# Performance work log

Measured on AMD Instinct MI355X. Metric: run time of the kernel, lower is better.

## Reference

```python
import jax, jax.numpy as jnp
import numpy as np

N = 100000
IN_DIM = 128
HID = 64
OUT = 4


def _gcn_conv(x, W, b, src, dst, deg_inv_sqrt):
    """PyG GCNConv: linear transform, then symmetric-normalized scatter-add.
    src/dst already include self-loops; deg_inv_sqrt precomputed over them."""
    h = x @ W                                   # [N, H]
    norm = deg_inv_sqrt[src] * deg_inv_sqrt[dst]  # [E+N]
    msg = h[src] * norm[:, None]                # gather + scale, [E+N, H]
    out = jax.ops.segment_sum(msg, dst, num_segments=N)  # scatter-add
    return out + b


def setup_inputs() -> dict:
    key = jax.random.key(0)
    ks = jax.random.split(key, 8)
    E = 1600000
    x = jax.random.normal(ks[0], (N, IN_DIM), dtype=jnp.float32)
    edge_index = jax.random.randint(ks[1], (2, E), 0, N, dtype=jnp.int32)
    # Glorot-ish init for weights
    W1 = jax.random.normal(ks[2], (IN_DIM, HID), dtype=jnp.float32) / np.sqrt(IN_DIM)
    b1 = jnp.zeros((HID,), dtype=jnp.float32)
    W2 = jax.random.normal(ks[3], (HID, HID), dtype=jnp.float32) / np.sqrt(HID)
    b2 = jnp.zeros((HID,), dtype=jnp.float32)
    Wfc = jax.random.normal(ks[4], (HID, OUT), dtype=jnp.float32) / np.sqrt(HID)
    bfc = jnp.zeros((OUT,), dtype=jnp.float32)
    return {"x": x, "edge_index": edge_index, "W1": W1, "b1": b1,
            "W2": W2, "b2": b2, "Wfc": Wfc, "bfc": bfc}


def reference(x, edge_index, W1, b1, W2, b2, Wfc, bfc):
    # Add self-loops (GCNConv default add_self_loops=True)
    loops = jnp.arange(N, dtype=edge_index.dtype)
    src = jnp.concatenate([edge_index[0], loops])
    dst = jnp.concatenate([edge_index[1], loops])
    # Symmetric normalization: deg computed at aggregation targets (dst)
    deg = jax.ops.segment_sum(jnp.ones_like(dst, dtype=x.dtype), dst,
                              num_segments=N)
    deg_inv_sqrt = jnp.where(deg > 0, jax.lax.rsqrt(deg), 0.0)

    h = _gcn_conv(x, W1, b1, src, dst, deg_inv_sqrt)
    h = jax.nn.relu(h)                 # dropout is identity in eval mode
    h = _gcn_conv(h, W2, b2, src, dst, deg_inv_sqrt)
    h = jax.nn.relu(h)
    return h @ Wfc + bfc               # [N, 4]
```

## Files before the change

### kernel.cpp

```cpp
#include <hip/hip_runtime.h>
#include <hip/hip_fp16.h>


#define BCAP 5120
#define BINB 512
#define CHUNK 3200
#define CAP  64
#define LCAP 32

typedef float v2f __attribute__((ext_vector_type(2)));
typedef _Float16 f16x8 __attribute__((ext_vector_type(8)));
typedef float f32x4 __attribute__((ext_vector_type(4)));

__global__ __launch_bounds__(256) void k_bin(const int* __restrict__ src,
                                             const int* __restrict__ dst, int e,
                                             int* bcur, unsigned* __restrict__ binned) {
    __shared__ unsigned ec[CHUNK];
    __shared__ unsigned short eb[CHUNK];
    __shared__ int lh[512], lbase[512], lr[512];
    int t = threadIdx.x;
    for (int i = t; i < 512; i += 256) { lh[i] = 0; lr[i] = 0; }
    __syncthreads();
    int chunk = (e + BINB - 1) / BINB;
    int lo = blockIdx.x * chunk;
    int hi = min(e, lo + chunk);
    for (int i = lo + t; i < hi; i += 256) {
        int d = dst[i];
        int b = d >> 8;
        ec[i - lo] = ((unsigned)src[i] << 8) | (unsigned)(d & 255);
        eb[i - lo] = (unsigned short)b;
        atomicAdd(&lh[b], 1);
    }
    __syncthreads();
    for (int i = t; i < 512; i += 256)
        lbase[i] = lh[i] ? atomicAdd(&bcur[i], lh[i]) : 0;
    __syncthreads();
    int cnt = hi - lo;
    for (int i = t; i < cnt; i += 256) {
        int b = eb[i];
        int r = lbase[b] + atomicAdd(&lr[b], 1);
        if (r < BCAP)
            binned[(size_t)b * BCAP + r] = ec[i];
    }
}

__global__ __launch_bounds__(256) void k_bk2_gemm1(
        const unsigned* __restrict__ binned, const int* __restrict__ bcur,
        int nbk, int* __restrict__ cnt, int* __restrict__ slots,
        const float* __restrict__ X, const float* __restrict__ W1,
        __half* __restrict__ Hh, int n) {
    __shared__ union {
        struct {
            int lists[256 * (LCAP + 1)];
            int lcnt[256];
        } k;
        struct {
            _Float16 As[128 * 136];
            _Float16 Bs[64 * 136];
        } g;
    } sm;

    int t = threadIdx.x;

    if ((int)blockIdx.x < nbk) {
        int b = blockIdx.x;
        int node0 = b << 8;
        size_t ebase = (size_t)b * BCAP;
        int ecnt = min(bcur[b], BCAP);
        sm.k.lcnt[t] = 0;
        __syncthreads();
        for (int j = t; j < ecnt; j += 256) {
            unsigned ed = binned[ebase + j];
            int ld = ed & 255u;
            int s  = (int)(ed >> 8);
            int r  = atomicAdd(&sm.k.lcnt[ld], 1);
            if (r < LCAP)
                sm.k.lists[ld * (LCAP + 1) + r] = s;
            else if (r < CAP)
                slots[((size_t)(node0 + ld) << 6) + r] = s;
        }
        __syncthreads();
        if (node0 + t < n) cnt[node0 + t] = sm.k.lcnt[t];
        for (int k = t; k < 256 * LCAP; k += 256) {
            int ld = k >> 5;
            int r  = k & (LCAP - 1);
            if (r < min(sm.k.lcnt[ld], LCAP) && node0 + ld < n)
                slots[((size_t)(node0 + ld) << 6) + r] =
                    sm.k.lists[ld * (LCAP + 1) + r];
        }
    } else {
        constexpr int K = 128, KP = 136;
        _Float16* As = sm.g.As;
        _Float16* Bs = sm.g.Bs;
        _Float16* H = (_Float16*)Hh;

        #pragma unroll
        for (int p = 0; p < 8; ++p) {
            int i = t + p * 256;
            int k = i >> 4, nn4 = (i & 15) << 2;
            float4 v = ((const float4*)W1)[i];
            Bs[(nn4 + 0) * KP + k] = (_Float16)v.x;
            Bs[(nn4 + 1) * KP + k] = (_Float16)v.y;
            Bs[(nn4 + 2) * KP + k] = (_Float16)v.z;
            Bs[(nn4 + 3) * KP + k] = (_Float16)v.w;
        }

        int row0 = ((int)blockIdx.x - nbk) * 128;
        #pragma unroll
        for (int p = 0; p < 8; ++p) {
            int gi  = t + p * 256;
            int row = gi >> 4, sg = gi & 15;
            int grow = row0 + row;
            float4 v0 = make_float4(0.f, 0.f, 0.f, 0.f), v1 = v0;
            if (grow < n) {
                v0 = *(const float4*)(X + (size_t)grow * K + sg * 8);
                v1 = *(const float4*)(X + (size_t)grow * K + sg * 8 + 4);
            }
            union { __half2 h[4]; float4 f; } u;
            u.h[0] = __floats2half2_rn(v0.x, v0.y);
            u.h[1] = __floats2half2_rn(v0.z, v0.w);
            u.h[2] = __floats2half2_rn(v1.x, v1.y);
            u.h[3] = __floats2half2_rn(v1.z, v1.w);
            *(float4*)(As + row * KP + sg * 8) = u.f;
        }
        __syncthreads();

        int wv   = t >> 6;
        int lane = t & 63;
        int m    = lane & 15;
        int quad = lane >> 4;
        int r0   = wv * 32;

        f32x4 acc[2][4] = {};
        #pragma unroll
        for (int kb = 0; kb < K / 32; ++kb) {
            f16x8 af0 = *(const f16x8*)(As + (r0 + m) * KP + quad * 8 + kb * 32);
            f16x8 af1 = *(const f16x8*)(As + (r0 + 16 + m) * KP + quad * 8 + kb * 32);
            #pragma unroll
            for (int nt = 0; nt < 4; ++nt) {
                f16x8 bf = *(const f16x8*)(Bs + (nt * 16 + m) * KP + quad * 8 + kb * 32);
                acc[0][nt] = __builtin_amdgcn_mfma_f32_16x16x32_f16(af0, bf, acc[0][nt], 0, 0, 0);
                acc[1][nt] = __builtin_amdgcn_mfma_f32_16x16x32_f16(af1, bf, acc[1][nt], 0, 0, 0);
            }
        }

        #pragma unroll
        for (int mt = 0; mt < 2; ++mt) {
            int gr[4];
            #pragma unroll
            for (int r = 0; r < 4; ++r)
                gr[r] = row0 + r0 + mt * 16 + quad * 4 + r;
            #pragma unroll
            for (int nt = 0; nt < 4; ++nt)
                #pragma unroll
                for (int r = 0; r < 4; ++r) {
                    if (gr[r] < n)
                        H[(size_t)gr[r] * 64 + nt * 16 + m] =
                            (_Float16)acc[mt][nt][r];
                    else if (gr[r] == n)
                        H[(size_t)n * 64 + nt * 16 + m] = (_Float16)0.f;
                }
        }
    }
}

__device__ inline void add_row(const __half* __restrict__ hp, int s, int c4,
                               v2f& lo, v2f& hi) {
    float2 raw = *(const float2*)(hp + (size_t)s * 64 + c4);
    const __half2* p = (const __half2*)&raw;
    float2 l = __half22float2(p[0]);
    float2 h = __half22float2(p[1]);
    lo += (v2f){ l.x, l.y };
    hi += (v2f){ h.x, h.y };
}

__device__ inline void fma_row(const __half* __restrict__ hp, int s, int c4,
                               float w, v2f& lo, v2f& hi) {
    float2 raw = *(const float2*)(hp + (size_t)s * 64 + c4);
    const __half2* p = (const __half2*)&raw;
    float2 l = __half22float2(p[0]);
    float2 h = __half22float2(p[1]);
    lo += w * (v2f){ l.x, l.y };
    hi += w * (v2f){ h.x, h.y };
}

__global__ __launch_bounds__(256) void k_gather_mm(const __half* __restrict__ hp,
                                                   const int* __restrict__ slots,
                                                   const int* __restrict__ cnt,
                                                   const float* __restrict__ bias,
                                                   const float* __restrict__ W2,
                                                   __half* __restrict__ h2,
                                                   int n) {
    int lane = threadIdx.x & 63;
    int wid  = (blockIdx.x * blockDim.x + threadIdx.x) >> 6;
    if (wid >= n) return;
    int d    = wid;
    int esub = lane >> 4;
    int c4   = (lane & 15) * 4;

    float w[64];
    #pragma unroll
    for (int k = 0; k < 64; ++k)
        w[k] = W2[k * 64 + lane];

    size_t start = (size_t)d << 6;
    int num = cnt[d];
    int lim = min(num, CAP);
    int idx = (lane < lim) ? slots[start + lane] : 0;
    float dsv = rsqrtf((float)(cnt[idx] + 1));
    float dd  = rsqrtf((float)(num + 1));

    v2f aL[4] = {}, aH[4] = {};
    if (esub == 0)
        fma_row(hp, d, c4, dd, aL[0], aH[0]);

    int j = 0;
    for (; j + 16 <= lim; j += 16) {
        int s0 = __shfl(idx, j + esub);
        int s1 = __shfl(idx, j + 4 + esub);
        int s2 = __shfl(idx, j + 8 + esub);
        int s3 = __shfl(idx, j + 12 + esub);
        float w0 = __shfl(dsv, j + esub);
        float w1 = __shfl(dsv, j + 4 + esub);
        float w2 = __shfl(dsv, j + 8 + esub);
        float w3 = __shfl(dsv, j + 12 + esub);
        fma_row(hp, s0, c4, w0, aL[0], aH[0]);
        fma_row(hp, s1, c4, w1, aL[1], aH[1]);
        fma_row(hp, s2, c4, w2, aL[2], aH[2]);
        fma_row(hp, s3, c4, w3, aL[3], aH[3]);
    }
    for (; j < lim; j += 4) {
        int jj = j + esub;
        int sr = __shfl(idx, jj);
        int s  = (jj < lim) ? sr : n;
        float ww = __shfl(dsv, jj);
        fma_row(hp, s, c4, ww, aL[0], aH[0]);
    }
    v2f sL = (aL[0] + aL[1]) + (aL[2] + aL[3]);
    v2f sH = (aH[0] + aH[1]) + (aH[2] + aH[3]);
    float4 a0 = make_float4(sL.x, sL.y, sH.x, sH.y);
    #pragma unroll
    for (int o = 16; o <= 32; o <<= 1) {
        a0.x += __shfl_xor(a0.x, o);
        a0.y += __shfl_xor(a0.y, o);
        a0.z += __shfl_xor(a0.z, o);
        a0.w += __shfl_xor(a0.w, o);
    }
    float4 bb = *(const float4*)(bias + c4);
    float4 o;
    o.x = fmaxf(bb.x + dd * a0.x, 0.f);
    o.y = fmaxf(bb.y + dd * a0.y, 0.f);
    o.z = fmaxf(bb.z + dd * a0.z, 0.f);
    o.w = fmaxf(bb.w + dd * a0.w, 0.f);

    float s = 0.f;
    #pragma unroll
    for (int kq = 0; kq < 16; ++kq) {
        float ax = __shfl(o.x, kq);
        float ay = __shfl(o.y, kq);
        float az = __shfl(o.z, kq);
        float aw = __shfl(o.w, kq);
        s += ax * w[4 * kq + 0];
        s += ay * w[4 * kq + 1];
        s += az * w[4 * kq + 2];
        s += aw * w[4 * kq + 3];
    }
    _Float16* h2f = (_Float16*)h2;
    h2f[(size_t)d * 64 + lane] = (_Float16)(s * dd);
    if (wid == 0)
        h2f[(size_t)n * 64 + lane] = (_Float16)0.f;
}

__global__ __launch_bounds__(256) void k_gather_fc(const __half* __restrict__ hp,
                                                   const int* __restrict__ slots,
                                                   const int* __restrict__ cnt,
                                                   const float* __restrict__ bias,
                                                   float* __restrict__ outb,
                                                   const float* __restrict__ Wfc,
                                                   const float* __restrict__ bfc,
                                                   int n) {
    int lane = threadIdx.x & 63;
    int wid  = (blockIdx.x * blockDim.x + threadIdx.x) >> 6;
    if (wid >= n) return;
    int d    = wid;
    int esub = lane >> 4;
    int c4   = (lane & 15) * 4;

    size_t start = (size_t)d << 6;
    int num = cnt[d];
    int lim = min(num, CAP);
    int idx = (lane < lim) ? slots[start + lane] : 0;
    float dd = rsqrtf((float)(num + 1));

    v2f aL[4] = {}, aH[4] = {};
    if (esub == 0)
        add_row(hp, d, c4, aL[0], aH[0]);

    int j = 0;
    for (; j + 16 <= lim; j += 16) {
        int s0 = __shfl(idx, j + esub);
        int s1 = __shfl(idx, j + 4 + esub);
        int s2 = __shfl(idx, j + 8 + esub);
        int s3 = __shfl(idx, j + 12 + esub);
        add_row(hp, s0, c4, aL[0], aH[0]);
        add_row(hp, s1, c4, aL[1], aH[1]);
        add_row(hp, s2, c4, aL[2], aH[2]);
        add_row(hp, s3, c4, aL[3], aH[3]);
    }
    for (; j < lim; j += 4) {
        int jj = j + esub;
        int sr = __shfl(idx, jj);
        int s  = (jj < lim) ? sr : n;
        add_row(hp, s, c4, aL[0], aH[0]);
    }
    v2f sL = (aL[0] + aL[1]) + (aL[2] + aL[3]);
    v2f sH = (aH[0] + aH[1]) + (aH[2] + aH[3]);
    float4 a0 = make_float4(sL.x, sL.y, sH.x, sH.y);
    #pragma unroll
    for (int o = 16; o <= 32; o <<= 1) {
        a0.x += __shfl_xor(a0.x, o);
        a0.y += __shfl_xor(a0.y, o);
        a0.z += __shfl_xor(a0.z, o);
        a0.w += __shfl_xor(a0.w, o);
    }
    float4 bb = *(const float4*)(bias + c4);
    float4 o;
    o.x = fmaxf(bb.x + dd * a0.x, 0.f);
    o.y = fmaxf(bb.y + dd * a0.y, 0.f);
    o.z = fmaxf(bb.z + dd * a0.z, 0.f);
    o.w = fmaxf(bb.w + dd * a0.w, 0.f);

    const float4* W4 = (const float4*)Wfc;
    float4 w0 = W4[c4 + 0], w1 = W4[c4 + 1], w2 = W4[c4 + 2], w3 = W4[c4 + 3];
    float4 p;
    p.x = o.x * w0.x + o.y * w1.x + o.z * w2.x + o.w * w3.x;
    p.y = o.x * w0.y + o.y * w1.y + o.z * w2.y + o.w * w3.y;
    p.z = o.x * w0.z + o.y * w1.z + o.z * w2.z + o.w * w3.z;
    p.w = o.x * w0.w + o.y * w1.w + o.z * w2.w + o.w * w3.w;
    #pragma unroll
    for (int q = 1; q <= 8; q <<= 1) {
        p.x += __shfl_xor(p.x, q);
        p.y += __shfl_xor(p.y, q);
        p.z += __shfl_xor(p.z, q);
        p.w += __shfl_xor(p.w, q);
    }
    if (lane == 0) {
        float4 bf = *(const float4*)bfc;
        float4 r = make_float4(p.x + bf.x, p.y + bf.y, p.z + bf.z, p.w + bf.w);
        ((float4*)outb)[d] = r;
    }
}

static inline size_t align256(size_t x) { return (x + 255) & ~(size_t)255; }

extern "C" void kernel_launch(void* const* d_in, const int* in_sizes, int n_in,
                              void* d_out, int out_size, void* d_ws, size_t ws_size,
                              hipStream_t stream) {
    const float* x   = (const float*)d_in[0];
    const int*   ei  = (const int*)d_in[1];
    const float* W1  = (const float*)d_in[2];
    const float* b1  = (const float*)d_in[3];
    const float* W2  = (const float*)d_in[4];
    const float* b2  = (const float*)d_in[5];
    const float* Wfc = (const float*)d_in[6];
    const float* bfc = (const float*)d_in[7];
    float* out = (float*)d_out;

    int n = in_sizes[0] / 128;
    int e = in_sizes[1] / 2;
    const int* src = ei;
    const int* dst = ei + e;

    char* ws = (char*)d_ws;
    size_t p = 0;
    int*      cnt    = (int*)     (ws + p); p = align256(p + (size_t)n * 4);
    int*      bcur   = (int*)     (ws + p); p = align256(p + 512 * 4);
    unsigned* binned = (unsigned*)(ws + p); p = align256(p + (size_t)512 * BCAP * 4);
    int*      slots  = (int*)     (ws + p); p = align256(p + (size_t)n * CAP * 4);
    __half*   hbuf   = (__half*)  (ws + p); p = align256(p + (size_t)(n + 1) * 64 * 2);
    __half*   hbuf2  = (__half*)  (ws + p); p = align256(p + (size_t)(n + 1) * 64 * 2);

    int gb  = (n + 127) / 128;
    int nbk = (n + 255) / 256;

    hipMemsetAsync(bcur, 0, 512 * sizeof(int), stream);
    k_bin<<<BINB, 256, 0, stream>>>(src, dst, e, bcur, binned);
    k_bk2_gemm1<<<nbk + gb, 256, 0, stream>>>(binned, bcur, nbk, cnt, slots,
                                              x, W1, hbuf, n);

    k_gather_mm<<<(n * 64 + 255) / 256, 256, 0, stream>>>(
        hbuf, slots, cnt, b1, W2, hbuf2, n);

    k_gather_fc<<<(n * 64 + 255) / 256, 256, 0, stream>>>(
        hbuf2, slots, cnt, b2, out, Wfc, bfc, n);
}
```

Baseline: 309.2 us.

## Fuse edge binning with GEMM1, use finer buckets, stage W2 in LDS

Moves the edge-binning pass into the same launch as the first GEMM so the two run concurrently. Bucket granularity drops from 256 to 128 destination nodes, giving 784 buckets and a separate 512-thread bucketing kernel. The gather-matmul kernel now stages a transposed W2 in shared memory instead of holding 64 weights per thread in registers, which is meant to cut register pressure and raise occupancy. The trade-offs are an extra block-wide barrier, LDS use, and a per-bucket capacity of 2560 edges, which could drop edges if a bucket overflows.

```diff
diff --git a/kernel.cpp b/kernel.cpp
--- a/kernel.cpp
+++ b/kernel.cpp
@@ -2,9 +2,10 @@
 #include <hip/hip_fp16.h>
 
 
-#define BCAP 5120
+#define BCAP 2560
 #define BINB 512
 #define CHUNK 3200
+#define NBH  784
 #define CAP  64
 #define LCAP 32
 
@@ -12,48 +13,17 @@
 typedef _Float16 f16x8 __attribute__((ext_vector_type(8)));
 typedef float f32x4 __attribute__((ext_vector_type(4)));
 
-__global__ __launch_bounds__(256) void k_bin(const int* __restrict__ src,
-                                             const int* __restrict__ dst, int e,
-                                             int* bcur, unsigned* __restrict__ binned) {
-    __shared__ unsigned ec[CHUNK];
-    __shared__ unsigned short eb[CHUNK];
-    __shared__ int lh[512], lbase[512], lr[512];
-    int t = threadIdx.x;
-    for (int i = t; i < 512; i += 256) { lh[i] = 0; lr[i] = 0; }
-    __syncthreads();
-    int chunk = (e + BINB - 1) / BINB;
-    int lo = blockIdx.x * chunk;
-    int hi = min(e, lo + chunk);
-    for (int i = lo + t; i < hi; i += 256) {
-        int d = dst[i];
-        int b = d >> 8;
-        ec[i - lo] = ((unsigned)src[i] << 8) | (unsigned)(d & 255);
-        eb[i - lo] = (unsigned short)b;
-        atomicAdd(&lh[b], 1);
-    }
-    __syncthreads();
-    for (int i = t; i < 512; i += 256)
-        lbase[i] = lh[i] ? atomicAdd(&bcur[i], lh[i]) : 0;
-    __syncthreads();
-    int cnt = hi - lo;
-    for (int i = t; i < cnt; i += 256) {
-        int b = eb[i];
-        int r = lbase[b] + atomicAdd(&lr[b], 1);
-        if (r < BCAP)
-            binned[(size_t)b * BCAP + r] = ec[i];
-    }
-}
-
-__global__ __launch_bounds__(256) void k_bk2_gemm1(
-        const unsigned* __restrict__ binned, const int* __restrict__ bcur,
-        int nbk, int* __restrict__ cnt, int* __restrict__ slots,
+__global__ __launch_bounds__(256) void k_bin_gemm1(
+        const int* __restrict__ src, const int* __restrict__ dst, int e,
+        int* bcur, unsigned* __restrict__ binned,
         const float* __restrict__ X, const float* __restrict__ W1,
         __half* __restrict__ Hh, int n) {
     __shared__ union {
         struct {
-            int lists[256 * (LCAP + 1)];
-            int lcnt[256];
-        } k;
+            unsigned ec[CHUNK];
+            unsigned short eb[CHUNK];
+            int lh[NBH], lbase[NBH], lr[NBH];
+        } b;
         struct {
             _Float16 As[128 * 136];
             _Float16 Bs[64 * 136];
@@ -62,31 +32,30 @@
 
     int t = threadIdx.x;
 
-    if ((int)blockIdx.x < nbk) {
-        int b = blockIdx.x;
-        int node0 = b << 8;
-        size_t ebase = (size_t)b * BCAP;
-        int ecnt = min(bcur[b], BCAP);
-        sm.k.lcnt[t] = 0;
+    if ((int)blockIdx.x < BINB) {
+        auto& B = sm.b;
+        for (int i = t; i < NBH; i += 256) { B.lh[i] = 0; B.lr[i] = 0; }
         __syncthreads();
-        for (int j = t; j < ecnt; j += 256) {
-            unsigned ed = binned[ebase + j];
-            int ld = ed & 255u;
-            int s  = (int)(ed >> 8);
-            int r  = atomicAdd(&sm.k.lcnt[ld], 1);
-            if (r < LCAP)
-                sm.k.lists[ld * (LCAP + 1) + r] = s;
-            else if (r < CAP)
-                slots[((size_t)(node0 + ld) << 6) + r] = s;
+        int chunk = (e + BINB - 1) / BINB;
+        int lo = blockIdx.x * chunk;
+        int hi = min(e, lo + chunk);
+        for (int i = lo + t; i < hi; i += 256) {
+            int d = dst[i];
+            int b = d >> 7;
+            B.ec[i - lo] = ((unsigned)src[i] << 7) | (unsigned)(d & 127);
+            B.eb[i - lo] = (unsigned short)b;
+            atomicAdd(&B.lh[b], 1);
         }
         __syncthreads();
-        if (node0 + t < n) cnt[node0 + t] = sm.k.lcnt[t];
-        for (int k = t; k < 256 * LCAP; k += 256) {
-            int ld = k >> 5;
-            int r  = k & (LCAP - 1);
-            if (r < min(sm.k.lcnt[ld], LCAP) && node0 + ld < n)
-                slots[((size_t)(node0 + ld) << 6) + r] =
-                    sm.k.lists[ld * (LCAP + 1) + r];
+        for (int i = t; i < NBH; i += 256)
+            B.lbase[i] = B.lh[i] ? atomicAdd(&bcur[i], B.lh[i]) : 0;
+        __syncthreads();
+        int cnt = hi - lo;
+        for (int i = t; i < cnt; i += 256) {
+            int b = B.eb[i];
+            int r = B.lbase[b] + atomicAdd(&B.lr[b], 1);
+            if (r < BCAP)
+                binned[(size_t)b * BCAP + r] = B.ec[i];
         }
     } else {
         constexpr int K = 128, KP = 136;
@@ -105,7 +74,7 @@
             Bs[(nn4 + 3) * KP + k] = (_Float16)v.w;
         }
 
-        int row0 = ((int)blockIdx.x - nbk) * 128;
+        int row0 = ((int)blockIdx.x - BINB) * 128;
         #pragma unroll
         for (int p = 0; p < 8; ++p) {
             int gi  = t + p * 256;
@@ -164,6 +133,39 @@
     }
 }
 
+__global__ __launch_bounds__(512) void k_bucket2(const unsigned* __restrict__ binned,
+                                                 const int* __restrict__ bcur,
+                                                 int n, int* __restrict__ cnt,
+                                                 int* __restrict__ slots) {
+    __shared__ int lists[128 * (LCAP + 1)];
+    __shared__ int lcnt[128];
+    int b = blockIdx.x, t = threadIdx.x;
+    int node0 = b << 7;
+    size_t ebase = (size_t)b * BCAP;
+    int ecnt = min(bcur[b], BCAP);
+    if (t < 128) lcnt[t] = 0;
+    __syncthreads();
+    for (int j = t; j < ecnt; j += 512) {
+        unsigned ed = binned[ebase + j];
+        int ld = ed & 127u;
+        int s  = (int)(ed >> 7);
+        int r  = atomicAdd(&lcnt[ld], 1);
+        if (r < LCAP)
+            lists[ld * (LCAP + 1) + r] = s;
+        else if (r < CAP)
+            slots[((size_t)(node0 + ld) << 6) + r] = s;
+    }
+    __syncthreads();
+    if (t < 128 && node0 + t < n) cnt[node0 + t] = lcnt[t];
+    for (int k = t; k < 128 * LCAP; k += 512) {
+        int ld = k >> 5;
+        int r  = k & (LCAP - 1);
+        if (r < min(lcnt[ld], LCAP) && node0 + ld < n)
+            slots[((size_t)(node0 + ld) << 6) + r] =
+                lists[ld * (LCAP + 1) + r];
+    }
+}
+
 __device__ inline void add_row(const __half* __restrict__ hp, int s, int c4,
                                v2f& lo, v2f& hi) {
     float2 raw = *(const float2*)(hp + (size_t)s * 64 + c4);
@@ -191,84 +193,100 @@
                                                    const float* __restrict__ W2,
                                                    __half* __restrict__ h2,
                                                    int n) {
-    int lane = threadIdx.x & 63;
-    int wid  = (blockIdx.x * blockDim.x + threadIdx.x) >> 6;
-    if (wid >= n) return;
-    int d    = wid;
+    __shared__ float W2s[64 * 65];
+    int t    = threadIdx.x;
+    int lane = t & 63;
+
+    #pragma unroll
+    for (int p = 0; p < 4; ++p) {
+        int i = t + p * 256;
+        int k = i >> 4, j0 = (i & 15) << 2;
+        float4 v = ((const float4*)W2)[i];
+        W2s[(j0 + 0) * 65 + k] = v.x;
+        W2s[(j0 + 1) * 65 + k] = v.y;
+        W2s[(j0 + 2) * 65 + k] = v.z;
+        W2s[(j0 + 3) * 65 + k] = v.w;
+    }
+
+    int wid  = (blockIdx.x * blockDim.x + t) >> 6;
+    bool active = wid < n;
+    int d    = active ? wid : 0;
     int esub = lane >> 4;
     int c4   = (lane & 15) * 4;
 
-    float w[64];
-    #pragma unroll
-    for (int k = 0; k < 64; ++k)
-        w[k] = W2[k * 64 + lane];
-
-    size_t start = (size_t)d << 6;
-    int num = cnt[d];
-    int lim = min(num, CAP);
-    int idx = (lane < lim) ? slots[start + lane] : 0;
-    float dsv = rsqrtf((float)(cnt[idx] + 1));
-    float dd  = rsqrtf((float)(num + 1));
-
-    v2f aL[4] = {}, aH[4] = {};
-    if (esub == 0)
-        fma_row(hp, d, c4, dd, aL[0], aH[0]);
-
-    int j = 0;
-    for (; j + 16 <= lim; j += 16) {
-        int s0 = __shfl(idx, j + esub);
-        int s1 = __shfl(idx, j + 4 + esub);
-        int s2 = __shfl(idx, j + 8 + esub);
-        int s3 = __shfl(idx, j + 12 + esub);
-        float w0 = __shfl(dsv, j + esub);
-        float w1 = __shfl(dsv, j + 4 + esub);
-        float w2 = __shfl(dsv, j + 8 + esub);
-        float w3 = __shfl(dsv, j + 12 + esub);
-        fma_row(hp, s0, c4, w0, aL[0], aH[0]);
-        fma_row(hp, s1, c4, w1, aL[1], aH[1]);
-        fma_row(hp, s2, c4, w2, aL[2], aH[2]);
-        fma_row(hp, s3, c4, w3, aL[3], aH[3]);
-    }
-    for (; j < lim; j += 4) {
-        int jj = j + esub;
-        int sr = __shfl(idx, jj);
-        int s  = (jj < lim) ? sr : n;
-        float ww = __shfl(dsv, jj);
-        fma_row(hp, s, c4, ww, aL[0], aH[0]);
-    }
-    v2f sL = (aL[0] + aL[1]) + (aL[2] + aL[3]);
-    v2f sH = (aH[0] + aH[1]) + (aH[2] + aH[3]);
-    float4 a0 = make_float4(sL.x, sL.y, sH.x, sH.y);
-    #pragma unroll
-    for (int o = 16; o <= 32; o <<= 1) {
-        a0.x += __shfl_xor(a0.x, o);
-        a0.y += __shfl_xor(a0.y, o);
-        a0.z += __shfl_xor(a0.z, o);
-        a0.w += __shfl_xor(a0.w, o);
-    }
-    float4 bb = *(const float4*)(bias + c4);
-    float4 o;
-    o.x = fmaxf(bb.x + dd * a0.x, 0.f);
-    o.y = fmaxf(bb.y + dd * a0.y, 0.f);
-    o.z = fmaxf(bb.z + dd * a0.z, 0.f);
-    o.w = fmaxf(bb.w + dd * a0.w, 0.f);
-
-    float s = 0.f;
-    #pragma unroll
-    for (int kq = 0; kq < 16; ++kq) {
-        float ax = __shfl(o.x, kq);
-        float ay = __shfl(o.y, kq);
-        float az = __shfl(o.z, kq);
-        float aw = __shfl(o.w, kq);
-        s += ax * w[4 * kq + 0];
-        s += ay * w[4 * kq + 1];
-        s += az * w[4 * kq + 2];
-        s += aw * w[4 * kq + 3];
-    }
-    _Float16* h2f = (_Float16*)h2;
-    h2f[(size_t)d * 64 + lane] = (_Float16)(s * dd);
-    if (wid == 0)
-        h2f[(size_t)n * 64 + lane] = (_Float16)0.f;
+    float dd = 0.f;
+    float4 o = make_float4(0.f, 0.f, 0.f, 0.f);
+    if (active) {
+        size_t start = (size_t)d << 6;
+        int num = cnt[d];
+        int lim = min(num, CAP);
+        int idx = (lane < lim) ? slots[start + lane] : 0;
+        float dsv = rsqrtf((float)(cnt[idx] + 1));
+        dd = rsqrtf((float)(num + 1));
+
+        v2f aL[4] = {}, aH[4] = {};
+        if (esub == 0)
+            fma_row(hp, d, c4, dd, aL[0], aH[0]);
+
+        int j = 0;
+        for (; j + 16 <= lim; j += 16) {
+            int s0 = __shfl(idx, j + esub);
+            int s1 = __shfl(idx, j + 4 + esub);
+            int s2 = __shfl(idx, j + 8 + esub);
+            int s3 = __shfl(idx, j + 12 + esub);
+            float w0 = __shfl(dsv, j + esub);
+            float w1 = __shfl(dsv, j + 4 + esub);
+            float w2 = __shfl(dsv, j + 8 + esub);
+            float w3 = __shfl(dsv, j + 12 + esub);
+            fma_row(hp, s0, c4, w0, aL[0], aH[0]);
+            fma_row(hp, s1, c4, w1, aL[1], aH[1]);
+            fma_row(hp, s2, c4, w2, aL[2], aH[2]);
+            fma_row(hp, s3, c4, w3, aL[3], aH[3]);
+        }
+        for (; j < lim; j += 4) {
+            int jj = j + esub;
+            int sr = __shfl(idx, jj);
+            int s  = (jj < lim) ? sr : n;
+            float w = __shfl(dsv, jj);
+            fma_row(hp, s, c4, w, aL[0], aH[0]);
+        }
+        v2f sL = (aL[0] + aL[1]) + (aL[2] + aL[3]);
+        v2f sH = (aH[0] + aH[1]) + (aH[2] + aH[3]);
+        float4 a0 = make_float4(sL.x, sL.y, sH.x, sH.y);
+        #pragma unroll
+        for (int q = 16; q <= 32; q <<= 1) {
+            a0.x += __shfl_xor(a0.x, q);
+            a0.y += __shfl_xor(a0.y, q);
+            a0.z += __shfl_xor(a0.z, q);
+            a0.w += __shfl_xor(a0.w, q);
+        }
+        float4 bb = *(const float4*)(bias + c4);
+        o.x = fmaxf(bb.x + dd * a0.x, 0.f);
+        o.y = fmaxf(bb.y + dd * a0.y, 0.f);
+        o.z = fmaxf(bb.z + dd * a0.z, 0.f);
+        o.w = fmaxf(bb.w + dd * a0.w, 0.f);
+    }
+
+    __syncthreads();
+
+    if (active) {
+        float s = 0.f;
+        #pragma unroll
+        for (int kq = 0; kq < 16; ++kq) {
+            float ax = __shfl(o.x, kq);
+            float ay = __shfl(o.y, kq);
+            float az = __shfl(o.z, kq);
+            float aw = __shfl(o.w, kq);
+            s += ax * W2s[lane * 65 + 4 * kq + 0];
+            s += ay * W2s[lane * 65 + 4 * kq + 1];
+            s += az * W2s[lane * 65 + 4 * kq + 2];
+            s += aw * W2s[lane * 65 + 4 * kq + 3];
+        }
+        _Float16* h2f = (_Float16*)h2;
+        h2f[(size_t)d * 64 + lane] = (_Float16)(s * dd);
+        if (wid == 0)
+            h2f[(size_t)n * 64 + lane] = (_Float16)0.f;
+    }
 }
 
 __global__ __launch_bounds__(256) void k_gather_fc(const __half* __restrict__ hp,
@@ -374,19 +392,19 @@
     char* ws = (char*)d_ws;
     size_t p = 0;
     int*      cnt    = (int*)     (ws + p); p = align256(p + (size_t)n * 4);
-    int*      bcur   = (int*)     (ws + p); p = align256(p + 512 * 4);
-    unsigned* binned = (unsigned*)(ws + p); p = align256(p + (size_t)512 * BCAP * 4);
+    int*      bcur   = (int*)     (ws + p); p = align256(p + NBH * 4);
+    unsigned* binned = (unsigned*)(ws + p); p = align256(p + (size_t)NBH * BCAP * 4);
     int*      slots  = (int*)     (ws + p); p = align256(p + (size_t)n * CAP * 4);
     __half*   hbuf   = (__half*)  (ws + p); p = align256(p + (size_t)(n + 1) * 64 * 2);
     __half*   hbuf2  = (__half*)  (ws + p); p = align256(p + (size_t)(n + 1) * 64 * 2);
 
     int gb  = (n + 127) / 128;
-    int nbk = (n + 255) / 256;
-
-    hipMemsetAsync(bcur, 0, 512 * sizeof(int), stream);
-    k_bin<<<BINB, 256, 0, stream>>>(src, dst, e, bcur, binned);
-    k_bk2_gemm1<<<nbk + gb, 256, 0, stream>>>(binned, bcur, nbk, cnt, slots,
-                                              x, W1, hbuf, n);
+    int nbk = (n + 127) / 128;
+
+    hipMemsetAsync(bcur, 0, NBH * sizeof(int), stream);
+    k_bin_gemm1<<<BINB + gb, 256, 0, stream>>>(src, dst, e, bcur, binned,
+                                               x, W1, hbuf, n);
+    k_bucket2<<<nbk, 512, 0, stream>>>(binned, bcur, n, cnt, slots);
 
     k_gather_mm<<<(n * 64 + 255) / 256, 256, 0, stream>>>(
         hbuf, slots, cnt, b1, W2, hbuf2, n);
```

After: 308.6 us. No clear change (-0.2%).
